# Kernel optimization log

Measured on AMD Instinct MI355X. Metric: run time of the kernel, lower is better.

The kernel has to match this reference:

```python
import jax, jax.numpy as jnp
import numpy as np

N = 512     # nodes
E = 16384   # edges (N * avg_degree 32, unique pairs)
F = 64      # nedgeinput
FO = 64     # nedgeoutput


def setup_inputs() -> dict:
    key = jax.random.key(0)
    ks = jax.random.split(key, 7)
    # unique edge pairs so scatter-assign is well-defined
    perm = jax.random.permutation(ks[0], N * N)[:E]
    edge_index = jnp.stack([perm // N, perm % N]).astype(jnp.int32)  # [2, E]
    C = jax.random.normal(ks[1], (E, F), dtype=jnp.float32)
    batch_node = jax.random.normal(ks[2], (N,), dtype=jnp.float32)
    s = 1.0 / np.sqrt(F)
    W_L1 = jax.random.normal(ks[3], (F, F), dtype=jnp.float32) * s          # Linear(F, F), weight [out,in]
    W_L2 = jax.random.normal(ks[4], (F, F), dtype=jnp.float32) * s
    W_mlp1 = jax.random.normal(ks[5], (8 * F, 2 * F), dtype=jnp.float32) * (1.0 / np.sqrt(2 * F))
    W_mlp2 = jax.random.normal(ks[6], (FO, 8 * F), dtype=jnp.float32) * (1.0 / np.sqrt(8 * F))
    return {"edge_index": edge_index, "C": C, "batch_node": batch_node,
            "W_L1": W_L1, "W_L2": W_L2, "W_mlp1": W_mlp1, "W_mlp2": W_mlp2}


def reference(edge_index, C, batch_node, W_L1, W_L2, W_mlp1, W_mlp2):
    n = batch_node.shape[0]
    f = C.shape[1]
    ei0, ei1 = edge_index[0], edge_index[1]
    X = C @ W_L1.T  # [E, F]  (L1(C))
    Y = C @ W_L2.T  # [E, F]  (L2(C))
    # scatter edges into dense [F, N, N] adjacency-like tensors
    resx = jnp.zeros((f, n, n), dtype=C.dtype).at[:, ei0, ei1].set(X.T)
    resy = jnp.zeros((f, n, n), dtype=C.dtype).at[:, ei0, ei1].set(Y.T)
    # batched dense matmul per feature channel, then gather back at edges
    res = jnp.einsum('fij,fjk->fik', resx, resy)  # [F, N, N]
    tmp_matmul = res[:, ei0, ei1].T  # [E, F]
    tmp = jnp.concatenate([C, tmp_matmul], axis=1)  # [E, 2F]
    return jax.nn.relu(tmp @ W_mlp1.T) @ W_mlp2.T  # [E, FO]
```

## Files before the change

kernel.cpp:

```cpp
#include <hip/hip_runtime.h>

#define NN 512
#define NE 16384
#define NF 64

typedef __attribute__((ext_vector_type(8))) short short8_t;
typedef __attribute__((ext_vector_type(4))) float float4_t;

__device__ inline unsigned short f2bf(float f) {
  unsigned u = __builtin_bit_cast(unsigned, f);
  u += 0x7fff + ((u >> 16) & 1);
  return (unsigned short)(u >> 16);
}
__device__ inline float bf2f(unsigned short u) {
  unsigned v = ((unsigned)u) << 16;
  return __builtin_bit_cast(float, v);
}

__global__ __launch_bounds__(256) void k_xy_mfma(const float* __restrict__ C,
                                                 const float* __restrict__ W1,
                                                 const float* __restrict__ W2,
                                                 const int* __restrict__ ei,
                                                 int* __restrict__ eid,
                                                 int* __restrict__ eidT,
                                                 unsigned* __restrict__ maskO,
                                                 unsigned* __restrict__ maskI,
                                                 unsigned short* __restrict__ Xb,
                                                 unsigned short* __restrict__ Yb) {
  __shared__ __attribute__((aligned(16))) short W1s[64 * 72];
  __shared__ __attribute__((aligned(16))) short W2s[64 * 72];
  int t = threadIdx.x;
  int w = t >> 6;
  int lane = t & 63;
  int col = lane & 15;
  int q = lane >> 4;
  int base_e = blockIdx.x * 64 + w * 16;

  if (t < 64) {
    int e = blockIdx.x * 64 + t;
    int i = ei[e];
    int k = ei[NE + e];
    eid[i * NN + k] = e;
    eidT[k * NN + i] = e;
    atomicOr(&maskO[i * 16 + (k >> 5)], 1u << (k & 31));
    atomicOr(&maskI[k * 16 + (i >> 5)], 1u << (i & 31));
  }

#pragma unroll
  for (int z = 0; z < 4; z++) {
    int gi = z * 256 + t;
    int r = gi >> 4, c = gi & 15;
    float4 v1 = ((const float4*)W1)[r * 16 + c];
    float4 v2 = ((const float4*)W2)[r * 16 + c];
    short4 s1, s2;
    s1.x = f2bf(v1.x); s1.y = f2bf(v1.y); s1.z = f2bf(v1.z); s1.w = f2bf(v1.w);
    s2.x = f2bf(v2.x); s2.y = f2bf(v2.y); s2.z = f2bf(v2.z); s2.w = f2bf(v2.w);
    *(short4*)(W1s + r * 72 + c * 4) = s1;
    *(short4*)(W2s + r * 72 + c * 4) = s2;
  }
  __syncthreads();

  short8_t bfrag[2];
#pragma unroll
  for (int ks = 0; ks < 2; ks++) {
    float4 c0 = ((const float4*)C)[(size_t)(base_e + col) * 16 + ks * 8 + q * 2];
    float4 c1 = ((const float4*)C)[(size_t)(base_e + col) * 16 + ks * 8 + q * 2 + 1];
    short8_t s;
    s[0] = (short)f2bf(c0.x); s[1] = (short)f2bf(c0.y);
    s[2] = (short)f2bf(c0.z); s[3] = (short)f2bf(c0.w);
    s[4] = (short)f2bf(c1.x); s[5] = (short)f2bf(c1.y);
    s[6] = (short)f2bf(c1.z); s[7] = (short)f2bf(c1.w);
    bfrag[ks] = s;
  }

  float4_t xa[4], ya[4];
#pragma unroll
  for (int ft = 0; ft < 4; ft++) {
    xa[ft] = (float4_t){0.f, 0.f, 0.f, 0.f};
    ya[ft] = (float4_t){0.f, 0.f, 0.f, 0.f};
  }
#pragma unroll
  for (int ks = 0; ks < 2; ks++) {
#pragma unroll
    for (int ft = 0; ft < 4; ft++) {
      short8_t a1 = *(const short8_t*)(W1s + (ft * 16 + col) * 72 + ks * 32 + q * 8);
      short8_t a2 = *(const short8_t*)(W2s + (ft * 16 + col) * 72 + ks * 32 + q * 8);
      xa[ft] = __builtin_amdgcn_mfma_f32_16x16x32_bf16(a1, bfrag[ks], xa[ft], 0, 0, 0);
      ya[ft] = __builtin_amdgcn_mfma_f32_16x16x32_bf16(a2, bfrag[ks], ya[ft], 0, 0, 0);
    }
  }
#pragma unroll
  for (int ft = 0; ft < 4; ft++) {
    short4 sx, sy;
    sx.x = (short)f2bf(xa[ft][0]); sx.y = (short)f2bf(xa[ft][1]);
    sx.z = (short)f2bf(xa[ft][2]); sx.w = (short)f2bf(xa[ft][3]);
    sy.x = (short)f2bf(ya[ft][0]); sy.y = (short)f2bf(ya[ft][1]);
    sy.z = (short)f2bf(ya[ft][2]); sy.w = (short)f2bf(ya[ft][3]);
    *(short4*)(Xb + (size_t)(base_e + col) * 64 + ft * 16 + q * 4) = sx;
    *(short4*)(Yb + (size_t)(base_e + col) * 64 + ft * 16 + q * 4) = sy;
  }
}

__global__ __launch_bounds__(256) void k_spmm(const int* __restrict__ ei,
                                              const int* __restrict__ eid,
                                              const int* __restrict__ eidT,
                                              const unsigned* __restrict__ maskO,
                                              const unsigned* __restrict__ maskI,
                                              const unsigned short* __restrict__ Xb,
                                              const unsigned short* __restrict__ Yb,
                                              const float* __restrict__ Wm1,
                                              const float* __restrict__ Wm2,
                                              unsigned short* __restrict__ W1B,
                                              unsigned short* __restrict__ W2B,
                                              unsigned short* __restrict__ tmpB) {
  if (blockIdx.x < 96) {
    int t4 = blockIdx.x * 256 + threadIdx.x;
    if (t4 < 16384) {
      float4 v = ((const float4*)Wm1)[t4];
      short4 s;
      s.x = f2bf(v.x); s.y = f2bf(v.y); s.z = f2bf(v.z); s.w = f2bf(v.w);
      ((short4*)W1B)[t4] = s;
    } else {
      int i = t4 - 16384;
      float4 v = ((const float4*)Wm2)[i];
      short4 s;
      s.x = f2bf(v.x); s.y = f2bf(v.y); s.z = f2bf(v.z); s.w = f2bf(v.w);
      ((short4*)W2B)[i] = s;
    }
  }

  int lane = threadIdx.x & 63;
  int e = (blockIdx.x * 256 + threadIdx.x) >> 6;
  int i = ei[e];
  int k = ei[NE + e];
  unsigned mm = 0;
  if (lane < 16) mm = maskO[i * 16 + lane] & maskI[k * 16 + lane];
  unsigned long long has = __ballot(mm != 0);
  float acc = 0.f;
  while (has) {
    int l = (int)__builtin_ctzll(has);
    has &= has - 1;
    unsigned bits = __shfl(mm, l);
    while (bits) {
      int b = __builtin_ctz(bits);
      bits &= bits - 1;
      int j = l * 32 + b;
      int s1 = eid[i * NN + j];
      int s2 = eidT[k * NN + j];
      float xv = bf2f(Xb[(size_t)s1 * 64 + lane]);
      float yv = bf2f(Yb[(size_t)s2 * 64 + lane]);
      acc = fmaf(xv, yv, acc);
    }
  }
  tmpB[(size_t)e * 128 + 64 + lane] = f2bf(acc);
}

__global__ __launch_bounds__(256) void k_mlp2(
    const float* __restrict__ C,
    const unsigned short* __restrict__ tmpB,
    const unsigned short* __restrict__ W1B,
    const unsigned short* __restrict__ W2B,
    float* __restrict__ out) {
  __shared__ __attribute__((aligned(16))) short W1s[128 * 136];
  __shared__ __attribute__((aligned(16))) short W2s[64 * 136];
  __shared__ __attribute__((aligned(16))) short hS[4][16 * 72];

  int t = threadIdx.x;
  int w = t >> 6;
  int lane = t & 63;
  int col = lane & 15;
  int q = lane >> 4;
  int g = w & 1;
  int h = w >> 1;
  int base_e = blockIdx.x * 32 + g * 16;

  short8_t btmp[4];
#pragma unroll
  for (int ks = 0; ks < 2; ks++) {
    float4 c0 = ((const float4*)C)[(size_t)(base_e + col) * 16 + ks * 8 + q * 2];
    float4 c1 = ((const float4*)C)[(size_t)(base_e + col) * 16 + ks * 8 + q * 2 + 1];
    short8_t s;
    s[0] = (short)f2bf(c0.x); s[1] = (short)f2bf(c0.y);
    s[2] = (short)f2bf(c0.z); s[3] = (short)f2bf(c0.w);
    s[4] = (short)f2bf(c1.x); s[5] = (short)f2bf(c1.y);
    s[6] = (short)f2bf(c1.z); s[7] = (short)f2bf(c1.w);
    btmp[ks] = s;
  }
#pragma unroll
  for (int ks = 2; ks < 4; ks++)
    btmp[ks] = *(const short8_t*)(tmpB + (size_t)(base_e + col) * 128 + ks * 32 + q * 8);

  float4_t oacc[4];
#pragma unroll
  for (int ft = 0; ft < 4; ft++) oacc[ft] = (float4_t){0.f, 0.f, 0.f, 0.f};

  for (int it = 0; it < 4; it++) {
    __syncthreads();
    {
      uint4* d1 = (uint4*)W1s;
      const uint4* s1 = (const uint4*)W1B;
#pragma unroll
      for (int z = 0; z < 8; z++) {
        int gi = z * 256 + t;
        int r = gi >> 4, c = gi & 15;
        int grow = ((r >> 6) * 4 + it) * 64 + (r & 63);
        d1[r * 17 + c] = s1[(size_t)grow * 16 + c];
      }
      uint4* d2 = (uint4*)W2s;
      const uint4* s2 = (const uint4*)W2B;
#pragma unroll
      for (int z = 0; z < 4; z++) {
        int gi = z * 256 + t;
        int r = gi >> 4, c = gi & 15;
        int gc = ((c >> 3) * 4 + it) * 8 + (c & 7);
        d2[r * 17 + c] = s2[(size_t)r * 64 + gc];
      }
    }
    __syncthreads();

#pragma unroll
    for (int ht = 0; ht < 4; ht++) {
      float4_t hacc = (float4_t){0.f, 0.f, 0.f, 0.f};
#pragma unroll
      for (int ks = 0; ks < 4; ks++) {
        short8_t af = *(const short8_t*)(W1s + (h * 64 + ht * 16 + col) * 136 + ks * 32 + q * 8);
        hacc = __builtin_amdgcn_mfma_f32_16x16x32_bf16(af, btmp[ks], hacc, 0, 0, 0);
      }
      short4 hp;
      hp.x = (short)f2bf(fmaxf(hacc[0], 0.f));
      hp.y = (short)f2bf(fmaxf(hacc[1], 0.f));
      hp.z = (short)f2bf(fmaxf(hacc[2], 0.f));
      hp.w = (short)f2bf(fmaxf(hacc[3], 0.f));
      *(short4*)(&hS[w][col * 72 + ht * 16 + q * 4]) = hp;
    }

#pragma unroll
    for (int ks2 = 0; ks2 < 2; ks2++) {
      short8_t a2 = *(const short8_t*)(&hS[w][col * 72 + ks2 * 32 + q * 8]);
#pragma unroll
      for (int ft = 0; ft < 4; ft++) {
        short8_t b2 = *(const short8_t*)(W2s + (ft * 16 + col) * 136 + h * 64 + ks2 * 32 + q * 8);
        oacc[ft] = __builtin_amdgcn_mfma_f32_16x16x32_bf16(a2, b2, oacc[ft], 0, 0, 0);
      }
    }
  }

  __syncthreads();
  float* red = (float*)W1s;
  if (h == 1) {
#pragma unroll
    for (int ft = 0; ft < 4; ft++)
#pragma unroll
      for (int r = 0; r < 4; r++)
        red[(g * 16 + q * 4 + r) * 66 + ft * 16 + col] = oacc[ft][r];
  }
  __syncthreads();
  if (h == 0) {
#pragma unroll
    for (int ft = 0; ft < 4; ft++)
#pragma unroll
      for (int r = 0; r < 4; r++) {
        float v = oacc[ft][r] + red[(g * 16 + q * 4 + r) * 66 + ft * 16 + col];
        out[(size_t)(base_e + q * 4 + r) * 64 + ft * 16 + col] = v;
      }
  }
}

extern "C" void kernel_launch(void* const* d_in, const int* in_sizes, int n_in,
                              void* d_out, int out_size, void* d_ws, size_t ws_size,
                              hipStream_t stream) {
  const int* ei = (const int*)d_in[0];
  const float* C = (const float*)d_in[1];
  const float* W1 = (const float*)d_in[3];
  const float* W2 = (const float*)d_in[4];
  const float* Wm1 = (const float*)d_in[5];
  const float* Wm2 = (const float*)d_in[6];
  float* out = (float*)d_out;

  char* p = (char*)d_ws;
  int* eid = (int*)p;                 p += (size_t)NN * NN * 4;
  int* eidT = (int*)p;                p += (size_t)NN * NN * 4;
  unsigned* masks = (unsigned*)p;     p += (size_t)16384 * 4;
  unsigned short* Xb = (unsigned short*)p;    p += (size_t)NE * NF * 2;
  unsigned short* Yb = (unsigned short*)p;    p += (size_t)NE * NF * 2;
  unsigned short* tmpB = (unsigned short*)p;  p += (size_t)NE * 128 * 2;
  unsigned short* W1B = (unsigned short*)p;   p += (size_t)512 * 128 * 2;
  unsigned short* W2B = (unsigned short*)p;   p += (size_t)64 * 512 * 2;
  unsigned* maskO = masks;
  unsigned* maskI = masks + 8192;

  hipMemsetAsync(masks, 0, 16384 * sizeof(unsigned), stream);
  k_xy_mfma<<<NE / 64, 256, 0, stream>>>(C, W1, W2, ei, eid, eidT, maskO, maskI, Xb, Yb);
  k_spmm<<<(NE * 64) / 256, 256, 0, stream>>>(ei, eid, eidT, maskO, maskI, Xb, Yb,
                                              Wm1, Wm2, W1B, W2B, tmpB);
  k_mlp2<<<NE / 32, 256, 0, stream>>>(C, tmpB, W1B, W2B, out);
}
```

Before: 97.51 us.

## Compact intersection indices in LDS and batch gathers eight-wide in spmm

The spmm kernel now turns each edge's mask intersection into a compact list of middle-node indices in shared memory, using a prefix scan over 16 lanes. It then loads eight index pairs and eight X/Y values before accumulating, so the dependent gathers overlap instead of running serially. The transposed eid table is dropped and the second index is read as eid[j*NN+k], which removes one scattered write and a buffer. The cost is a block-wide sync, 8 KB of LDS per block and padded dummy loads. Column-strided eid reads are also less cache-friendly.

```diff
diff --git a/kernel.cpp b/kernel.cpp
--- a/kernel.cpp
+++ b/kernel.cpp
@@ -22,7 +22,6 @@
                                                  const float* __restrict__ W2,
                                                  const int* __restrict__ ei,
                                                  int* __restrict__ eid,
-                                                 int* __restrict__ eidT,
                                                  unsigned* __restrict__ maskO,
                                                  unsigned* __restrict__ maskI,
                                                  unsigned short* __restrict__ Xb,
@@ -41,7 +40,6 @@
     int i = ei[e];
     int k = ei[NE + e];
     eid[i * NN + k] = e;
-    eidT[k * NN + i] = e;
     atomicOr(&maskO[i * 16 + (k >> 5)], 1u << (k & 31));
     atomicOr(&maskI[k * 16 + (i >> 5)], 1u << (i & 31));
   }
@@ -103,7 +101,6 @@
 
 __global__ __launch_bounds__(256) void k_spmm(const int* __restrict__ ei,
                                               const int* __restrict__ eid,
-                                              const int* __restrict__ eidT,
                                               const unsigned* __restrict__ maskO,
                                               const unsigned* __restrict__ maskI,
                                               const unsigned short* __restrict__ Xb,
@@ -113,6 +110,13 @@
                                               unsigned short* __restrict__ W1B,
                                               unsigned short* __restrict__ W2B,
                                               unsigned short* __restrict__ tmpB) {
+  __shared__ int jl[4][512];
+  int lane = threadIdx.x & 63;
+  int w = threadIdx.x >> 6;
+  int e = (blockIdx.x * 256 + threadIdx.x) >> 6;
+  int i = ei[e];
+  int k = ei[NE + e];
+
   if (blockIdx.x < 96) {
     int t4 = blockIdx.x * 256 + threadIdx.x;
     if (t4 < 16384) {
@@ -121,35 +125,56 @@
       s.x = f2bf(v.x); s.y = f2bf(v.y); s.z = f2bf(v.z); s.w = f2bf(v.w);
       ((short4*)W1B)[t4] = s;
     } else {
-      int i = t4 - 16384;
-      float4 v = ((const float4*)Wm2)[i];
+      int i2 = t4 - 16384;
+      float4 v = ((const float4*)Wm2)[i2];
       short4 s;
       s.x = f2bf(v.x); s.y = f2bf(v.y); s.z = f2bf(v.z); s.w = f2bf(v.w);
-      ((short4*)W2B)[i] = s;
-    }
-  }
-
-  int lane = threadIdx.x & 63;
-  int e = (blockIdx.x * 256 + threadIdx.x) >> 6;
-  int i = ei[e];
-  int k = ei[NE + e];
+      ((short4*)W2B)[i2] = s;
+    }
+  }
+
   unsigned mm = 0;
   if (lane < 16) mm = maskO[i * 16 + lane] & maskI[k * 16 + lane];
-  unsigned long long has = __ballot(mm != 0);
+
+  int mcnt = __popc(mm);
+  int incl = mcnt;
+#pragma unroll
+  for (int d = 1; d < 16; d <<= 1) {
+    int y = __shfl_up(incl, d);
+    if (lane >= d) incl += y;
+  }
+  int off = incl - mcnt;
+  int cnt = __shfl(incl, 15);
+  unsigned bits = mm;
+  while (bits) {
+    int b = __builtin_ctz(bits);
+    bits &= bits - 1;
+    jl[w][off++] = lane * 32 + b;
+  }
+  __syncthreads();
+
   float acc = 0.f;
-  while (has) {
-    int l = (int)__builtin_ctzll(has);
-    has &= has - 1;
-    unsigned bits = __shfl(mm, l);
-    while (bits) {
-      int b = __builtin_ctz(bits);
-      bits &= bits - 1;
-      int j = l * 32 + b;
-      int s1 = eid[i * NN + j];
-      int s2 = eidT[k * NN + j];
-      float xv = bf2f(Xb[(size_t)s1 * 64 + lane]);
-      float yv = bf2f(Yb[(size_t)s2 * 64 + lane]);
-      acc = fmaf(xv, yv, acc);
+  for (int base = 0; base < cnt; base += 8) {
+    int idx[8], s1[8], s2[8];
+#pragma unroll
+    for (int b = 0; b < 8; b++) {
+      int t = base + b;
+      idx[b] = jl[w][t < cnt ? t : base];
+    }
+#pragma unroll
+    for (int b = 0; b < 8; b++) {
+      s1[b] = eid[i * NN + idx[b]];
+      s2[b] = eid[idx[b] * NN + k];
+    }
+    float xv[8], yv[8];
+#pragma unroll
+    for (int b = 0; b < 8; b++) {
+      xv[b] = bf2f(Xb[(size_t)s1[b] * 64 + lane]);
+      yv[b] = bf2f(Yb[(size_t)s2[b] * 64 + lane]);
+    }
+#pragma unroll
+    for (int b = 0; b < 8; b++) {
+      if (base + b < cnt) acc = fmaf(xv[b], yv[b], acc);
     }
   }
   tmpB[(size_t)e * 128 + 64 + lane] = f2bf(acc);
@@ -279,7 +304,6 @@
 
   char* p = (char*)d_ws;
   int* eid = (int*)p;                 p += (size_t)NN * NN * 4;
-  int* eidT = (int*)p;                p += (size_t)NN * NN * 4;
   unsigned* masks = (unsigned*)p;     p += (size_t)16384 * 4;
   unsigned short* Xb = (unsigned short*)p;    p += (size_t)NE * NF * 2;
   unsigned short* Yb = (unsigned short*)p;    p += (size_t)NE * NF * 2;
@@ -290,8 +314,8 @@
   unsigned* maskI = masks + 8192;
 
   hipMemsetAsync(masks, 0, 16384 * sizeof(unsigned), stream);
-  k_xy_mfma<<<NE / 64, 256, 0, stream>>>(C, W1, W2, ei, eid, eidT, maskO, maskI, Xb, Yb);
-  k_spmm<<<(NE * 64) / 256, 256, 0, stream>>>(ei, eid, eidT, maskO, maskI, Xb, Yb,
+  k_xy_mfma<<<NE / 64, 256, 0, stream>>>(C, W1, W2, ei, eid, maskO, maskI, Xb, Yb);
+  k_spmm<<<(NE * 64) / 256, 256, 0, stream>>>(ei, eid, maskO, maskI, Xb, Yb,
                                               Wm1, Wm2, W1B, W2B, tmpB);
   k_mlp2<<<NE / 32, 256, 0, stream>>>(C, tmpB, W1B, W2B, out);
 }
```

Measured after the change: 96.46 us. Within noise of the previous version (-1.1%).
